# Performance work log

Hardware: AMD Instinct MI355X
Metric: run time of the kernel (lower is better)

## Reference

```python
import jax, jax.numpy as jnp
import numpy as np

DIM = 1024
HEADS = 16
HEAD_DIM = DIM // HEADS
EPS = 1e-5  # torch LayerNorm default


def layer_norm(x, w, b):
    mu = jnp.mean(x, axis=-1, keepdims=True)
    var = jnp.mean(jnp.square(x - mu), axis=-1, keepdims=True)
    return (x - mu) * jax.lax.rsqrt(var + EPS) * w + b


def apply_rope(x, pos):
    # x: [B, H, N, D], pos: [N] int32. Standard 1D rotary, split-half style.
    d2 = x.shape[-1] // 2
    inv_freq = 1.0 / (10000.0 ** (jnp.arange(d2, dtype=jnp.float32) / d2))
    ang = pos.astype(jnp.float32)[:, None] * inv_freq[None, :]  # [N, D/2]
    cos, sin = jnp.cos(ang), jnp.sin(ang)
    x1, x2 = x[..., :d2], x[..., d2:]
    return jnp.concatenate([x1 * cos - x2 * sin, x1 * sin + x2 * cos], axis=-1)


def setup_inputs() -> dict:
    key = jax.random.key(0)
    ks = jax.random.split(key, 8)
    B, N, C = 2, 2048, DIM
    s = 1.0 / np.sqrt(C)
    return {
        "x": jax.random.normal(ks[0], (B, N, C), dtype=jnp.float32),
        "qkv_w": jax.random.normal(ks[1], (3 * C, C), dtype=jnp.float32) * s,
        "qn_w": jnp.ones((HEAD_DIM,), jnp.float32),
        "qn_b": jnp.zeros((HEAD_DIM,), jnp.float32),
        "kn_w": jnp.ones((HEAD_DIM,), jnp.float32),
        "kn_b": jnp.zeros((HEAD_DIM,), jnp.float32),
        "proj_w": jax.random.normal(ks[2], (C, C), dtype=jnp.float32) * s,
        "proj_b": jnp.zeros((C,), jnp.float32),
        "pos": jnp.arange(N, dtype=jnp.int32),
    }


def reference(x, qkv_w, qn_w, qn_b, kn_w, kn_b, proj_w, proj_b, pos):
    B, N, C = x.shape
    H, D = HEADS, HEAD_DIM
    scale = D ** -0.5
    qkv = jnp.einsum('bnc,oc->bno', x, qkv_w).reshape(B, N, 3, H, D)
    qkv = jnp.moveaxis(qkv, (2, 3), (0, 2))  # [3, B, H, N, D]
    q, k, v = qkv[0], qkv[1], qkv[2]
    q = layer_norm(q, qn_w, qn_b)
    k = layer_norm(k, kn_w, kn_b)
    q = apply_rope(q, pos)
    k = apply_rope(k, pos)
    attn = jax.nn.softmax(jnp.einsum('bhqd,bhkd->bhqk', q * scale, k), axis=-1)
    out = jnp.einsum('bhqk,bhkd->bhqd', attn, v)  # [B, H, N, D]
    out = out.transpose(0, 2, 1, 3).reshape(B, N, C)
    return jnp.einsum('bnc,oc->bno', out, proj_w) + proj_b
```

## Files before the change

kernel.cpp:

```cpp
#include <hip/hip_runtime.h>
#include <hip/hip_bf16.h>
#include <math.h>
#include <stdint.h>

#define B 2
#define N 2048
#define C 1024
#define H 16
#define D 64
#define LN_EPS 1e-5f

typedef unsigned short u16;
typedef unsigned int u32;
typedef __attribute__((ext_vector_type(8))) short b16x8;
typedef __attribute__((ext_vector_type(4))) float f32x4;

#define MFMA(a, b, c) __builtin_amdgcn_mfma_f32_16x16x32_bf16(a, b, c, 0, 0, 0)

__device__ __forceinline__ u16 f2bf(float x) {
    u32 u = __float_as_uint(x);
    u32 r = u + 0x7fff + ((u >> 16) & 1);
    return (u16)(r >> 16);
}
__device__ __forceinline__ float bf2f(u16 v) {
    return __uint_as_float(((u32)v) << 16);
}
__device__ __forceinline__ void gload_lds16(const void* g, void* l) {
    __builtin_amdgcn_global_load_lds(
        (__attribute__((address_space(1))) void*)(uintptr_t)g,
        (__attribute__((address_space(3))) void*)l, 16, 0, 0);
}
__device__ __forceinline__ float exp2_asm(float x) {
    float r;
    asm("v_exp_f32 %0, %1" : "=v"(r) : "v"(x));
    return r;
}
__device__ __forceinline__ u32 cvtpk_bf16(float lo, float hi) {
    u32 r;
    asm("v_cvt_pk_bf16_f32 %0, %1, %2" : "=v"(r) : "v"(lo), "v"(hi));
    return r;
}

union PW { u32 w[4]; b16x8 v; };

__global__ __launch_bounds__(256) void castk3(
    const float* __restrict__ a, u16* __restrict__ oa, int na4,
    const float* __restrict__ b, u16* __restrict__ ob, int nb4,
    const float* __restrict__ c, u16* __restrict__ oc, int nc4,
    float* __restrict__ ropetab, const int* __restrict__ pos)
{
    int i = blockIdx.x * 256 + threadIdx.x;
    const float* src; u16* dst; int off;
    if (i < na4) { src = a; dst = oa; off = i; }
    else if (i < na4 + nb4) { src = b; dst = ob; off = i - na4; }
    else if (i < na4 + nb4 + nc4) { src = c; dst = oc; off = i - na4 - nb4; }
    else {
        const int idx = i - (na4 + nb4 + nc4);
        if (idx < N * 32) {
            const int nn = idx >> 5, d2 = idx & 31;
            const float invf = exp2_asm((float)d2 * -0.41524101186092029f);
            const float ang = (float)pos[nn] * invf;
            float2 cs;
            cs.x = cosf(ang);
            cs.y = sinf(ang);
            *(float2*)&ropetab[2 * idx] = cs;
        }
        return;
    }
    float4 v = ((const float4*)src)[off];
    ushort4 o;
    o.x = f2bf(v.x); o.y = f2bf(v.y); o.z = f2bf(v.z); o.w = f2bf(v.w);
    ((ushort4*)dst)[off] = o;
}

template <int MODE, int NFR>
__global__ __launch_bounds__(256) void mfma_gemm(
    const u16* __restrict__ A, const u16* __restrict__ W,
    float* __restrict__ outp, const float* __restrict__ bias,
    u16* __restrict__ qkb, u16* __restrict__ vbuf,
    const float* __restrict__ qnw, const float* __restrict__ qnb,
    const float* __restrict__ knw, const float* __restrict__ knb,
    const float* __restrict__ ropetab, int K)
{
    __shared__ u16 As[2][128 * 32];
    __shared__ u16 Ws[2][1024 * NFR];
    const int tid = threadIdx.x;
    const int lane = tid & 63, wave = tid >> 6;
    const int g = lane >> 4, c = lane & 15;
    const int wr = wave >> 1, wc = wave & 1;
    const int row0 = blockIdx.y * 128, col0 = blockIdx.x * (32 * NFR);

    f32x4 acc[4][NFR];
    #pragma unroll
    for (int m = 0; m < 4; ++m)
        #pragma unroll
        for (int n = 0; n < NFR; ++n) acc[m][n] = (f32x4){0.f, 0.f, 0.f, 0.f};

    auto stage = [&](int k0, int bi) {
        #pragma unroll
        for (int rep = 0; rep < 2; ++rep) {
            const int idx = rep * 256 + tid;
            const int r_ = idx >> 2, ch = idx & 3;
            gload_lds16(A + (size_t)(row0 + r_) * K + k0 + ch * 8,
                        As[bi] + rep * 2048 + wave * 512);
        }
        #pragma unroll
        for (int rep = 0; rep < NFR / 2; ++rep) {
            const int idx = rep * 256 + tid;
            const int r_ = idx >> 2, ch = idx & 3;
            gload_lds16(W + (size_t)(col0 + r_) * K + k0 + ch * 8,
                        Ws[bi] + rep * 2048 + wave * 512);
        }
    };

    stage(0, 0);
    __syncthreads();
    const int nt = K / 32;
    for (int t = 0; t < nt; ++t) {
        const int bi = t & 1;
        if (t + 1 < nt) stage((t + 1) * 32, bi ^ 1);

        b16x8 af[4], wf[NFR];
        #pragma unroll
        for (int m = 0; m < 4; ++m)
            af[m] = *(const b16x8*)&As[bi][(wr * 64 + m * 16 + c) * 32 + g * 8];
        #pragma unroll
        for (int n = 0; n < NFR; ++n)
            wf[n] = *(const b16x8*)&Ws[bi][(wc * 16 * NFR + n * 16 + c) * 32 + g * 8];
        #pragma unroll
        for (int m = 0; m < 4; ++m)
            #pragma unroll
            for (int n = 0; n < NFR; ++n)
                acc[m][n] = MFMA(af[m], wf[n], acc[m][n]);
        __syncthreads();
    }

    if (MODE == 0) {
        const int colbase = col0 + wc * 64;
        const int which = colbase >> 10;
        const int hh = (colbase >> 6) & (H - 1);
        if (which == 2) {
            #pragma unroll
            for (int m = 0; m < 4; ++m)
                #pragma unroll
                for (int n = 0; n < NFR; ++n)
                    #pragma unroll
                    for (int r = 0; r < 4; ++r) {
                        const int row = row0 + wr * 64 + m * 16 + g * 4 + r;
                        const int bb = row >> 11, nn = row & (N - 1);
                        vbuf[(((size_t)(bb * H + hh)) * N + nn) * 64 + n * 16 + c] =
                            f2bf(acc[m][n][r]);
                    }
        } else {
            const float* wv = which ? knw : qnw;
            const float* bv = which ? knb : qnb;
            float wl[4], bl[4];
            #pragma unroll
            for (int n = 0; n < 4; ++n) { wl[n] = wv[n * 16 + c]; bl[n] = bv[n * 16 + c]; }
            const float qs = which ? 1.0f : 0.18033688011112042f;
            u16* dst = qkb + (size_t)which * (B * H * N * D);
            #pragma unroll
            for (int m = 0; m < 4; ++m)
                #pragma unroll
                for (int r = 0; r < 4; ++r) {
                    const float v0 = acc[m][0][r], v1 = acc[m][1][r];
                    const float v2 = acc[m][2][r], v3 = acc[m][3][r];
                    float s = (v0 + v1) + (v2 + v3);
                    s += __shfl_xor(s, 1, 64); s += __shfl_xor(s, 2, 64);
                    s += __shfl_xor(s, 4, 64); s += __shfl_xor(s, 8, 64);
                    const float mu = s * (1.0f / 64.0f);
                    const float d0 = v0 - mu, d1 = v1 - mu;
                    const float d2_ = v2 - mu, d3 = v3 - mu;
                    float s2 = (d0 * d0 + d1 * d1) + (d2_ * d2_ + d3 * d3);
                    s2 += __shfl_xor(s2, 1, 64); s2 += __shfl_xor(s2, 2, 64);
                    s2 += __shfl_xor(s2, 4, 64); s2 += __shfl_xor(s2, 8, 64);
                    const float rstd = rsqrtf(s2 * (1.0f / 64.0f) + LN_EPS);
                    const float y0 = d0 * rstd * wl[0] + bl[0];
                    const float y1 = d1 * rstd * wl[1] + bl[1];
                    const float y2 = d2_ * rstd * wl[2] + bl[2];
                    const float y3 = d3 * rstd * wl[3] + bl[3];
                    const int row = row0 + wr * 64 + m * 16 + g * 4 + r;
                    const int bb = row >> 11, nn = row & (N - 1);
                    const float2 csa = *(const float2*)&ropetab[(size_t)nn * 64 + 2 * c];
                    const float2 csb = *(const float2*)&ropetab[(size_t)nn * 64 + 2 * (16 + c)];
                    const float o0 = (y0 * csa.x - y2 * csa.y) * qs;
                    const float o2 = (y0 * csa.y + y2 * csa.x) * qs;
                    const float o1 = (y1 * csb.x - y3 * csb.y) * qs;
                    const float o3 = (y1 * csb.y + y3 * csb.x) * qs;
                    u16* rp = dst + (((size_t)(bb * H + hh)) * N + nn) * 64;
                    rp[0 * 16 + c] = f2bf(o0);
                    rp[1 * 16 + c] = f2bf(o1);
                    rp[2 * 16 + c] = f2bf(o2);
                    rp[3 * 16 + c] = f2bf(o3);
                }
        }
    } else {
        #pragma unroll
        for (int m = 0; m < 4; ++m)
            #pragma unroll
            for (int n = 0; n < NFR; ++n)
                #pragma unroll
                for (int r = 0; r < 4; ++r) {
                    const int row = row0 + wr * 64 + m * 16 + g * 4 + r;
                    const int col = col0 + wc * 16 * NFR + n * 16 + c;
                    outp[(size_t)row * C + col] = acc[m][n][r] + bias[col];
                }
    }
}

__global__ __launch_bounds__(512, 2) void attn_kernel(
    const u16* __restrict__ qkb, const u16* __restrict__ vb, u16* __restrict__ aout)
{
    __shared__ u16 Kl[2][64 * 64];
    __shared__ u16 Vt[2][64 * 64];
    const int tid = threadIdx.x, lane = tid & 63, wave = tid >> 6;
    const int g = lane >> 4, c = lane & 15;
    const int p_ = blockIdx.x;
    const int bid = (p_ & 7) * 64 + (p_ >> 3);
    const int qt = bid & 15, h = (bid >> 4) & 15, b = bid >> 8;
    const size_t headbase = ((size_t)(b * H + h)) * N * D;
    const u16* Qg = qkb + headbase;
    const u16* Kg = qkb + (size_t)(B * H * N * D) + headbase;
    const u16* Vg = vb + headbase;
    const int q0 = qt * 128 + wave * 16;

    b16x8 qf[2];
    #pragma unroll
    for (int ks = 0; ks < 2; ++ks)
        qf[ks] = *(const b16x8*)&Qg[(size_t)(q0 + c) * 64 + ks * 32 + g * 8];

    f32x4 oacc[4];
    #pragma unroll
    for (int nd = 0; nd < 4; ++nd) oacc[nd] = (f32x4){0.f, 0.f, 0.f, 0.f};
    float l_run = 0.f;

    auto stageK = [&](int kt, int bi) {
        const int j = tid >> 3, cc2 = tid & 7;
        const int cg = cc2 ^ (j & 7);
        gload_lds16(Kg + (size_t)(kt * 64 + j) * 64 + cg * 8,
                    (u16*)Kl[bi] + (size_t)tid * 8);
    };

    const int vjp = (tid & 31) * 2;
    const int vdg = (tid >> 5) & 7;
    const int vddh = tid >> 8;
    const int vchunk16 = 4 * (vjp >> 5) + ((vjp >> 2) & 3);
    const int vpos = 4 * ((vjp >> 4) & 1) + (vjp & 3);
    ushort4 vA4, vB4;
    auto loadV = [&](int kt) {
        vA4 = *(const ushort4*)&Vg[(size_t)(kt * 64 + vjp) * 64 + vdg * 8 + vddh * 4];
        vB4 = *(const ushort4*)&Vg[(size_t)(kt * 64 + vjp + 1) * 64 + vdg * 8 + vddh * 4];
    };
    auto writeV = [&](int bi) {
        const u16 a_[4] = {vA4.x, vA4.y, vA4.z, vA4.w};
        const u16 b_[4] = {vB4.x, vB4.y, vB4.z, vB4.w};
        #pragma unroll
        for (int i = 0; i < 4; ++i) {
            const int dd = vddh * 4 + i;
            const int d = vdg * 8 + dd;
            const u32 pk = (u32)a_[i] | ((u32)b_[i] << 16);
            *(u32*)((char*)Vt[bi] + d * 128 + ((vchunk16 ^ dd) << 4) + vpos * 2) = pk;
        }
    };

    auto compute = [&](int bi) {
        const char* Kb = (const char*)Kl[bi];
        const char* Vb = (const char*)Vt[bi];
        f32x4 s[4];
        #pragma unroll
        for (int jt = 0; jt < 4; ++jt) s[jt] = (f32x4){0.f, 0.f, 0.f, 0.f};
        __builtin_amdgcn_s_setprio(1);
        #pragma unroll
        for (int jt = 0; jt < 4; ++jt)
            #pragma unroll
            for (int ks = 0; ks < 2; ++ks) {
                const int byteoff = (jt * 16 + c) * 128 + ((ks * 64 + g * 16) ^ ((c & 7) << 4));
                const b16x8 kf = *(const b16x8*)(Kb + byteoff);
                s[jt] = MFMA(kf, qf[ks], s[jt]);
            }
        __builtin_amdgcn_s_setprio(0);

        float psj[4];
        #pragma unroll
        for (int jt = 0; jt < 4; ++jt) {
            #pragma unroll
            for (int r = 0; r < 4; ++r) s[jt][r] = exp2_asm(s[jt][r]);
            psj[jt] = (s[jt][0] + s[jt][1]) + (s[jt][2] + s[jt][3]);
        }
        float ps = (psj[0] + psj[1]) + (psj[2] + psj[3]);
        ps += __shfl_xor(ps, 16, 64);
        ps += __shfl_xor(ps, 32, 64);
        l_run += ps;

        PW pw[2];
        #pragma unroll
        for (int ks = 0; ks < 2; ++ks)
            #pragma unroll
            for (int wd = 0; wd < 4; ++wd)
                pw[ks].w[wd] = cvtpk_bf16(s[2 * ks + (wd >> 1)][2 * (wd & 1)],
                                          s[2 * ks + (wd >> 1)][2 * (wd & 1) + 1]);

        __builtin_amdgcn_s_setprio(1);
        #pragma unroll
        for (int Dg = 0; Dg < 4; ++Dg) {
            #pragma unroll
            for (int kh = 0; kh < 2; ++kh) {
                const b16x8 vf = *(const b16x8*)(Vb + Dg * 2048 + c * 128 +
                                                 (((4 * kh + g) ^ (c & 7)) << 4));
                oacc[Dg] = MFMA(vf, pw[kh].v, oacc[Dg]);
            }
        }
        __builtin_amdgcn_s_setprio(0);
    };

    stageK(0, 0);
    loadV(0);
    writeV(0);
    __syncthreads();

    for (int kt = 0; kt < N / 64 - 1; ++kt) {
        const int bi = kt & 1;
        loadV(kt + 1);
        stageK(kt + 1, bi ^ 1);
        compute(bi);
        writeV(bi ^ 1);
        __syncthreads();
    }
    compute((N / 64 - 1) & 1);

    const float li = 1.0f / l_run;
    #pragma unroll
    for (int Dg = 0; Dg < 4; ++Dg) {
        uint2 pr;
        pr.x = cvtpk_bf16(oacc[Dg][0] * li, oacc[Dg][1] * li);
        pr.y = cvtpk_bf16(oacc[Dg][2] * li, oacc[Dg][3] * li);
        *(uint2*)&aout[((size_t)(b * N + q0 + c)) * C + h * 64 + Dg * 16 + g * 4] = pr;
    }
}

extern "C" void kernel_launch(void* const* d_in, const int* in_sizes, int n_in,
                              void* d_out, int out_size, void* d_ws, size_t ws_size,
                              hipStream_t stream) {
    const float* x      = (const float*)d_in[0];
    const float* qkv_w  = (const float*)d_in[1];
    const float* qn_w   = (const float*)d_in[2];
    const float* qn_b   = (const float*)d_in[3];
    const float* kn_w   = (const float*)d_in[4];
    const float* kn_b   = (const float*)d_in[5];
    const float* proj_w = (const float*)d_in[6];
    const float* proj_b = (const float*)d_in[7];
    const int*   pos    = (const int*)d_in[8];
    float* out = (float*)d_out;

    u16* xb      = (u16*)d_ws;
    u16* wqkvb   = xb + 4194304;
    u16* wprojb  = wqkvb + 3145728;
    u16* qkb     = wprojb + 1048576;
    u16* vbuf    = qkb + 8388608;
    u16* aob     = vbuf + 4194304;
    float* rtab  = (float*)(aob + 4194304);

    castk3<<<8448, 256, 0, stream>>>(x, xb, 1048576,
                                     qkv_w, wqkvb, 786432,
                                     proj_w, wprojb, 262144,
                                     rtab, pos);

    mfma_gemm<0, 4><<<dim3(24, 32), 256, 0, stream>>>(
        xb, wqkvb, nullptr, nullptr, qkb, vbuf,
        qn_w, qn_b, kn_w, kn_b, rtab, C);
    attn_kernel<<<512, 512, 0, stream>>>(qkb, vbuf, aob);
    mfma_gemm<1, 2><<<dim3(16, 32), 256, 0, stream>>>(
        aob, wprojb, out, proj_b, nullptr, nullptr,
        nullptr, nullptr, nullptr, nullptr, nullptr, C);
}
```

Baseline: 137.6 us.

## Process two query tiles per wave in attention to reuse K/V fragments

The attention kernel drops from 8 to 4 waves per block, and each wave now handles 32 query rows as two 16-row tiles. Every K and V fragment read from LDS feeds two MFMAs, which halves LDS read traffic per query. K staging and V transposition are redone so 256 threads cover the tile, with wider 16-byte V loads. This raises register pressure from doubled accumulators and score tiles, and fewer waves per block may reduce latency hiding.

```diff
diff --git a/kernel.cpp b/kernel.cpp
--- a/kernel.cpp
+++ b/kernel.cpp
@@ -208,7 +208,7 @@
     }
 }
 
-__global__ __launch_bounds__(512, 2) void attn_kernel(
+__global__ __launch_bounds__(256, 4) void attn_kernel(
     const u16* __restrict__ qkb, const u16* __restrict__ vb, u16* __restrict__ aout)
 {
     __shared__ u16 Kl[2][64 * 64];
@@ -222,43 +222,47 @@
     const u16* Qg = qkb + headbase;
     const u16* Kg = qkb + (size_t)(B * H * N * D) + headbase;
     const u16* Vg = vb + headbase;
-    const int q0 = qt * 128 + wave * 16;
-
-    b16x8 qf[2];
+    const int q0 = qt * 128 + wave * 32;
+
+    b16x8 qf[2][2];
     #pragma unroll
-    for (int ks = 0; ks < 2; ++ks)
-        qf[ks] = *(const b16x8*)&Qg[(size_t)(q0 + c) * 64 + ks * 32 + g * 8];
-
-    f32x4 oacc[4];
+    for (int qb_ = 0; qb_ < 2; ++qb_)
+        #pragma unroll
+        for (int ks = 0; ks < 2; ++ks)
+            qf[qb_][ks] = *(const b16x8*)&Qg[(size_t)(q0 + qb_ * 16 + c) * 64 + ks * 32 + g * 8];
+
+    f32x4 oacc[2][4];
     #pragma unroll
-    for (int nd = 0; nd < 4; ++nd) oacc[nd] = (f32x4){0.f, 0.f, 0.f, 0.f};
-    float l_run = 0.f;
+    for (int qb_ = 0; qb_ < 2; ++qb_)
+        #pragma unroll
+        for (int nd = 0; nd < 4; ++nd) oacc[qb_][nd] = (f32x4){0.f, 0.f, 0.f, 0.f};
+    float l_run[2] = {0.f, 0.f};
 
     auto stageK = [&](int kt, int bi) {
-        const int j = tid >> 3, cc2 = tid & 7;
-        const int cg = cc2 ^ (j & 7);
-        gload_lds16(Kg + (size_t)(kt * 64 + j) * 64 + cg * 8,
-                    (u16*)Kl[bi] + (size_t)tid * 8);
+        #pragma unroll
+        for (int rep = 0; rep < 2; ++rep) {
+            const int idx = rep * 256 + tid;
+            const int j = idx >> 3, cc2 = idx & 7;
+            const int cg = cc2 ^ (j & 7);
+            gload_lds16(Kg + (size_t)(kt * 64 + j) * 64 + cg * 8,
+                        (u16*)Kl[bi] + rep * 2048 + wave * 512);
+        }
     };
 
     const int vjp = (tid & 31) * 2;
-    const int vdg = (tid >> 5) & 7;
-    const int vddh = tid >> 8;
+    const int vdg = tid >> 5;
     const int vchunk16 = 4 * (vjp >> 5) + ((vjp >> 2) & 3);
     const int vpos = 4 * ((vjp >> 4) & 1) + (vjp & 3);
-    ushort4 vA4, vB4;
+    b16x8 vA8, vB8;
     auto loadV = [&](int kt) {
-        vA4 = *(const ushort4*)&Vg[(size_t)(kt * 64 + vjp) * 64 + vdg * 8 + vddh * 4];
-        vB4 = *(const ushort4*)&Vg[(size_t)(kt * 64 + vjp + 1) * 64 + vdg * 8 + vddh * 4];
+        vA8 = *(const b16x8*)&Vg[(size_t)(kt * 64 + vjp) * 64 + vdg * 8];
+        vB8 = *(const b16x8*)&Vg[(size_t)(kt * 64 + vjp + 1) * 64 + vdg * 8];
     };
     auto writeV = [&](int bi) {
-        const u16 a_[4] = {vA4.x, vA4.y, vA4.z, vA4.w};
-        const u16 b_[4] = {vB4.x, vB4.y, vB4.z, vB4.w};
-        #pragma unroll
-        for (int i = 0; i < 4; ++i) {
-            const int dd = vddh * 4 + i;
+        #pragma unroll
+        for (int dd = 0; dd < 8; ++dd) {
             const int d = vdg * 8 + dd;
-            const u32 pk = (u32)a_[i] | ((u32)b_[i] << 16);
+            const u32 pk = (u32)(u16)vA8[dd] | ((u32)(u16)vB8[dd] << 16);
             *(u32*)((char*)Vt[bi] + d * 128 + ((vchunk16 ^ dd) << 4) + vpos * 2) = pk;
         }
     };
@@ -266,9 +270,12 @@
     auto compute = [&](int bi) {
         const char* Kb = (const char*)Kl[bi];
         const char* Vb = (const char*)Vt[bi];
-        f32x4 s[4];
-        #pragma unroll
-        for (int jt = 0; jt < 4; ++jt) s[jt] = (f32x4){0.f, 0.f, 0.f, 0.f};
+        f32x4 s0[4], s1[4];
+        #pragma unroll
+        for (int jt = 0; jt < 4; ++jt) {
+            s0[jt] = (f32x4){0.f, 0.f, 0.f, 0.f};
+            s1[jt] = (f32x4){0.f, 0.f, 0.f, 0.f};
+        }
         __builtin_amdgcn_s_setprio(1);
         #pragma unroll
         for (int jt = 0; jt < 4; ++jt)
@@ -276,29 +283,50 @@
             for (int ks = 0; ks < 2; ++ks) {
                 const int byteoff = (jt * 16 + c) * 128 + ((ks * 64 + g * 16) ^ ((c & 7) << 4));
                 const b16x8 kf = *(const b16x8*)(Kb + byteoff);
-                s[jt] = MFMA(kf, qf[ks], s[jt]);
+                s0[jt] = MFMA(kf, qf[0][ks], s0[jt]);
+                s1[jt] = MFMA(kf, qf[1][ks], s1[jt]);
             }
         __builtin_amdgcn_s_setprio(0);
 
-        float psj[4];
-        #pragma unroll
-        for (int jt = 0; jt < 4; ++jt) {
-            #pragma unroll
-            for (int r = 0; r < 4; ++r) s[jt][r] = exp2_asm(s[jt][r]);
-            psj[jt] = (s[jt][0] + s[jt][1]) + (s[jt][2] + s[jt][3]);
-        }
-        float ps = (psj[0] + psj[1]) + (psj[2] + psj[3]);
-        ps += __shfl_xor(ps, 16, 64);
-        ps += __shfl_xor(ps, 32, 64);
-        l_run += ps;
-
-        PW pw[2];
-        #pragma unroll
-        for (int ks = 0; ks < 2; ++ks)
-            #pragma unroll
-            for (int wd = 0; wd < 4; ++wd)
-                pw[ks].w[wd] = cvtpk_bf16(s[2 * ks + (wd >> 1)][2 * (wd & 1)],
-                                          s[2 * ks + (wd >> 1)][2 * (wd & 1) + 1]);
+        PW pw0[2], pw1[2];
+        {
+            float psj[4];
+            #pragma unroll
+            for (int jt = 0; jt < 4; ++jt) {
+                #pragma unroll
+                for (int r = 0; r < 4; ++r) s0[jt][r] = exp2_asm(s0[jt][r]);
+                psj[jt] = (s0[jt][0] + s0[jt][1]) + (s0[jt][2] + s0[jt][3]);
+            }
+            float ps = (psj[0] + psj[1]) + (psj[2] + psj[3]);
+            ps += __shfl_xor(ps, 16, 64);
+            ps += __shfl_xor(ps, 32, 64);
+            l_run[0] += ps;
+            #pragma unroll
+            for (int ks = 0; ks < 2; ++ks)
+                #pragma unroll
+                for (int wd = 0; wd < 4; ++wd)
+                    pw0[ks].w[wd] = cvtpk_bf16(s0[2 * ks + (wd >> 1)][2 * (wd & 1)],
+                                               s0[2 * ks + (wd >> 1)][2 * (wd & 1) + 1]);
+        }
+        {
+            float psj[4];
+            #pragma unroll
+            for (int jt = 0; jt < 4; ++jt) {
+                #pragma unroll
+                for (int r = 0; r < 4; ++r) s1[jt][r] = exp2_asm(s1[jt][r]);
+                psj[jt] = (s1[jt][0] + s1[jt][1]) + (s1[jt][2] + s1[jt][3]);
+            }
+            float ps = (psj[0] + psj[1]) + (psj[2] + psj[3]);
+            ps += __shfl_xor(ps, 16, 64);
+            ps += __shfl_xor(ps, 32, 64);
+            l_run[1] += ps;
+            #pragma unroll
+            for (int ks = 0; ks < 2; ++ks)
+                #pragma unroll
+                for (int wd = 0; wd < 4; ++wd)
+                    pw1[ks].w[wd] = cvtpk_bf16(s1[2 * ks + (wd >> 1)][2 * (wd & 1)],
+                                               s1[2 * ks + (wd >> 1)][2 * (wd & 1) + 1]);
+        }
 
         __builtin_amdgcn_s_setprio(1);
         #pragma unroll
@@ -307,7 +335,8 @@
             for (int kh = 0; kh < 2; ++kh) {
                 const b16x8 vf = *(const b16x8*)(Vb + Dg * 2048 + c * 128 +
                                                  (((4 * kh + g) ^ (c & 7)) << 4));
-                oacc[Dg] = MFMA(vf, pw[kh].v, oacc[Dg]);
+                oacc[0][Dg] = MFMA(vf, pw0[kh].v, oacc[0][Dg]);
+                oacc[1][Dg] = MFMA(vf, pw1[kh].v, oacc[1][Dg]);
             }
         }
         __builtin_amdgcn_s_setprio(0);
@@ -328,13 +357,17 @@
     }
     compute((N / 64 - 1) & 1);
 
-    const float li = 1.0f / l_run;
     #pragma unroll
-    for (int Dg = 0; Dg < 4; ++Dg) {
-        uint2 pr;
-        pr.x = cvtpk_bf16(oacc[Dg][0] * li, oacc[Dg][1] * li);
-        pr.y = cvtpk_bf16(oacc[Dg][2] * li, oacc[Dg][3] * li);
-        *(uint2*)&aout[((size_t)(b * N + q0 + c)) * C + h * 64 + Dg * 16 + g * 4] = pr;
+    for (int qb_ = 0; qb_ < 2; ++qb_) {
+        const float li = 1.0f / l_run[qb_];
+        #pragma unroll
+        for (int Dg = 0; Dg < 4; ++Dg) {
+            uint2 pr;
+            pr.x = cvtpk_bf16(oacc[qb_][Dg][0] * li, oacc[qb_][Dg][1] * li);
+            pr.y = cvtpk_bf16(oacc[qb_][Dg][2] * li, oacc[qb_][Dg][3] * li);
+            *(uint2*)&aout[((size_t)(b * N + q0 + qb_ * 16 + c)) * C +
+                           h * 64 + Dg * 16 + g * 4] = pr;
+        }
     }
 }
 
@@ -368,7 +401,7 @@
     mfma_gemm<0, 4><<<dim3(24, 32), 256, 0, stream>>>(
         xb, wqkvb, nullptr, nullptr, qkb, vbuf,
         qn_w, qn_b, kn_w, kn_b, rtab, C);
-    attn_kernel<<<512, 512, 0, stream>>>(qkb, vbuf, aob);
+    attn_kernel<<<512, 256, 0, stream>>>(qkb, vbuf, aob);
     mfma_gemm<1, 2><<<dim3(16, 32), 256, 0, stream>>>(
         aob, wprojb, out, proj_b, nullptr, nullptr,
         nullptr, nullptr, nullptr, nullptr, nullptr, C);
```

New measurement: 159.0 us. 15.6% more time.

## Stage two K/V tiles per barrier and defer softmax row-sum reduction

Applied to the files above, without the earlier changes.

The attention loop now loads and stages two 64-key tiles per iteration into doubled shared-memory buffers, halving the number of __syncthreads barriers across the key sequence. The cross-lane shuffle reduction of the softmax denominator is moved out of the inner loop and done once at the end on a per-lane partial sum. The cost is double the LDS footprint (64 KB per block), which may limit two blocks per CU, plus extra registers for the second V prefetch.

```diff
diff --git a/kernel.cpp b/kernel.cpp
--- a/kernel.cpp
+++ b/kernel.cpp
@@ -211,8 +211,8 @@
 __global__ __launch_bounds__(512, 2) void attn_kernel(
     const u16* __restrict__ qkb, const u16* __restrict__ vb, u16* __restrict__ aout)
 {
-    __shared__ u16 Kl[2][64 * 64];
-    __shared__ u16 Vt[2][64 * 64];
+    __shared__ u16 Kl[2][2][64 * 64];
+    __shared__ u16 Vt[2][2][64 * 64];
     const int tid = threadIdx.x, lane = tid & 63, wave = tid >> 6;
     const int g = lane >> 4, c = lane & 15;
     const int p_ = blockIdx.x;
@@ -232,13 +232,13 @@
     f32x4 oacc[4];
     #pragma unroll
     for (int nd = 0; nd < 4; ++nd) oacc[nd] = (f32x4){0.f, 0.f, 0.f, 0.f};
-    float l_run = 0.f;
-
-    auto stageK = [&](int kt, int bi) {
+    float l_part = 0.f;
+
+    auto stageK = [&](int kt, u16* dstbuf) {
         const int j = tid >> 3, cc2 = tid & 7;
         const int cg = cc2 ^ (j & 7);
         gload_lds16(Kg + (size_t)(kt * 64 + j) * 64 + cg * 8,
-                    (u16*)Kl[bi] + (size_t)tid * 8);
+                    dstbuf + (size_t)tid * 8);
     };
 
     const int vjp = (tid & 31) * 2;
@@ -246,26 +246,31 @@
     const int vddh = tid >> 8;
     const int vchunk16 = 4 * (vjp >> 5) + ((vjp >> 2) & 3);
     const int vpos = 4 * ((vjp >> 4) & 1) + (vjp & 3);
-    ushort4 vA4, vB4;
-    auto loadV = [&](int kt) {
-        vA4 = *(const ushort4*)&Vg[(size_t)(kt * 64 + vjp) * 64 + vdg * 8 + vddh * 4];
-        vB4 = *(const ushort4*)&Vg[(size_t)(kt * 64 + vjp + 1) * 64 + vdg * 8 + vddh * 4];
-    };
-    auto writeV = [&](int bi) {
-        const u16 a_[4] = {vA4.x, vA4.y, vA4.z, vA4.w};
-        const u16 b_[4] = {vB4.x, vB4.y, vB4.z, vB4.w};
-        #pragma unroll
-        for (int i = 0; i < 4; ++i) {
-            const int dd = vddh * 4 + i;
-            const int d = vdg * 8 + dd;
-            const u32 pk = (u32)a_[i] | ((u32)b_[i] << 16);
-            *(u32*)((char*)Vt[bi] + d * 128 + ((vchunk16 ^ dd) << 4) + vpos * 2) = pk;
-        }
-    };
-
-    auto compute = [&](int bi) {
-        const char* Kb = (const char*)Kl[bi];
-        const char* Vb = (const char*)Vt[bi];
+    ushort4 vA4[2], vB4[2];
+    auto loadV2 = [&](int pair) {
+        #pragma unroll
+        for (int t = 0; t < 2; ++t) {
+            const int kt = 2 * pair + t;
+            vA4[t] = *(const ushort4*)&Vg[(size_t)(kt * 64 + vjp) * 64 + vdg * 8 + vddh * 4];
+            vB4[t] = *(const ushort4*)&Vg[(size_t)(kt * 64 + vjp + 1) * 64 + vdg * 8 + vddh * 4];
+        }
+    };
+    auto writeV2 = [&](int bi) {
+        #pragma unroll
+        for (int t = 0; t < 2; ++t) {
+            const u16 a_[4] = {vA4[t].x, vA4[t].y, vA4[t].z, vA4[t].w};
+            const u16 b_[4] = {vB4[t].x, vB4[t].y, vB4[t].z, vB4[t].w};
+            #pragma unroll
+            for (int i = 0; i < 4; ++i) {
+                const int dd = vddh * 4 + i;
+                const int d = vdg * 8 + dd;
+                const u32 pk = (u32)a_[i] | ((u32)b_[i] << 16);
+                *(u32*)((char*)Vt[bi][t] + d * 128 + ((vchunk16 ^ dd) << 4) + vpos * 2) = pk;
+            }
+        }
+    };
+
+    auto compute = [&](const char* Kb, const char* Vb) {
         f32x4 s[4];
         #pragma unroll
         for (int jt = 0; jt < 4; ++jt) s[jt] = (f32x4){0.f, 0.f, 0.f, 0.f};
@@ -287,10 +292,7 @@
             for (int r = 0; r < 4; ++r) s[jt][r] = exp2_asm(s[jt][r]);
             psj[jt] = (s[jt][0] + s[jt][1]) + (s[jt][2] + s[jt][3]);
         }
-        float ps = (psj[0] + psj[1]) + (psj[2] + psj[3]);
-        ps += __shfl_xor(ps, 16, 64);
-        ps += __shfl_xor(ps, 32, 64);
-        l_run += ps;
+        l_part += (psj[0] + psj[1]) + (psj[2] + psj[3]);
 
         PW pw[2];
         #pragma unroll
@@ -313,22 +315,33 @@
         __builtin_amdgcn_s_setprio(0);
     };
 
-    stageK(0, 0);
-    loadV(0);
-    writeV(0);
+    loadV2(0);
+    stageK(0, (u16*)Kl[0][0]);
+    stageK(1, (u16*)Kl[0][1]);
+    writeV2(0);
     __syncthreads();
 
-    for (int kt = 0; kt < N / 64 - 1; ++kt) {
-        const int bi = kt & 1;
-        loadV(kt + 1);
-        stageK(kt + 1, bi ^ 1);
-        compute(bi);
-        writeV(bi ^ 1);
+    const int npair = N / 128;
+    for (int p = 0; p < npair - 1; ++p) {
+        const int bi = p & 1;
+        loadV2(p + 1);
+        stageK(2 * p + 2, (u16*)Kl[bi ^ 1][0]);
+        stageK(2 * p + 3, (u16*)Kl[bi ^ 1][1]);
+        compute((const char*)Kl[bi][0], (const char*)Vt[bi][0]);
+        compute((const char*)Kl[bi][1], (const char*)Vt[bi][1]);
+        writeV2(bi ^ 1);
         __syncthreads();
     }
-    compute((N / 64 - 1) & 1);
-
-    const float li = 1.0f / l_run;
+    {
+        const int bi = (npair - 1) & 1;
+        compute((const char*)Kl[bi][0], (const char*)Vt[bi][0]);
+        compute((const char*)Kl[bi][1], (const char*)Vt[bi][1]);
+    }
+
+    float l = l_part;
+    l += __shfl_xor(l, 16, 64);
+    l += __shfl_xor(l, 32, 64);
+    const float li = 1.0f / l;
     #pragma unroll
     for (int Dg = 0; Dg < 4; ++Dg) {
         uint2 pr;
```

Result: no change. 136.1 us (-1.1%).
